# Performance work log

Hardware: AMD Instinct MI355X
Metric: run time of the kernel (lower is better)

## Reference

```python
import jax, jax.numpy as jnp
import numpy as np

N = 50000      # nodes
E = 800000     # edges (avg degree 16)
IN, HID, OUT = 256, 128, 64
K, ALPHA = 4, 0.0  # APPNPConv(k=4, alpha=0.0)


def setup_inputs() -> dict:
    key = jax.random.key(0)
    ks = jax.random.split(key, 5)
    features = jax.random.normal(ks[0], (N, IN), jnp.float32)
    src = jax.random.randint(ks[1], (E,), 0, N, jnp.int32)
    dst = jax.random.randint(ks[2], (E,), 0, N, jnp.int32)
    W1 = jax.random.normal(ks[3], (IN, HID), jnp.float32) / np.float32(np.sqrt(IN))
    b1 = jnp.zeros((HID,), jnp.float32)
    W3 = jax.random.normal(ks[4], (HID, OUT), jnp.float32) / np.float32(np.sqrt(HID))
    b3 = jnp.zeros((OUT,), jnp.float32)
    return dict(features=features, src=src, dst=dst, W1=W1, b1=b1, W3=W3, b3=b3)


def _sym_norms(src, dst, n):
    # D_out^{-1/2} for source side, D_in^{-1/2} for destination side (DGL norm='both')
    ones = jnp.ones((src.shape[0],), jnp.float32)
    deg_out = jax.ops.segment_sum(ones, src, num_segments=n)
    deg_in = jax.ops.segment_sum(ones, dst, num_segments=n)
    return jnp.clip(deg_out, 1.0) ** -0.5, jnp.clip(deg_in, 1.0) ** -0.5


def _prop(x, src, dst, norm_src, norm_dst):
    # x: [N, D]. Symmetric-normalized SpMM: D_in^{-1/2} A D_out^{-1/2} x
    msg = (x * norm_src[:, None])[src]                       # [E, D] gather
    agg = jax.ops.segment_sum(msg, dst, num_segments=x.shape[0])  # [N, D] scatter-add
    return agg * norm_dst[:, None]


def reference(features, src, dst, W1, b1, W3, b3):
    ns, nd = _sym_norms(src, dst, N)
    # GraphConv 1 (weight-first since in_dim > hidden_dim; math identical either way)
    h = _prop(features @ W1, src, dst, ns, nd) + b1
    # dropout is identity in eval mode (training=False)
    # APPNPConv: k=4 power-iteration steps with teleport alpha=0.0
    h0 = h
    for _ in range(K):
        h = (1.0 - ALPHA) * _prop(h, src, dst, ns, nd) + ALPHA * h0
    # GraphConv 3
    out = _prop(h @ W3, src, dst, ns, nd) + b3
    return out
```

## Files before the change

### kernel.cpp

```cpp
#include <hip/hip_runtime.h>
#include <math.h>

#define N_NODES 50000
#define N_EDGES 800000
#define DIN 256
#define DHID 128
#define DOUT 64
#define CSTRIDE 64
#define ZROW N_NODES
#define HBLOCKS 256
#define HCHUNK (N_EDGES / HBLOCKS)
#define HWORDS (N_NODES / 4)
#define SLICE ((size_t)(N_NODES + 1) * 16)
#define NGROUPS (N_NODES / 4)
#define P2BLOCKS 196

#define SB_SENT 3125
#define SB_HS (SB_SENT + HBLOCKS)
#define SB_HD (SB_HS + HBLOCKS)
#define SB_TOT (SB_HD + 66)

__global__ void k_setup(const int* __restrict__ src, const int* __restrict__ dst,
                        unsigned int* __restrict__ pS, unsigned int* __restrict__ pD,
                        unsigned int* __restrict__ csr32,
                        const float* __restrict__ W1, const float* __restrict__ b1,
                        const float* __restrict__ W3,
                        float* __restrict__ W13, float* __restrict__ bb,
                        float* __restrict__ Y0, float* __restrict__ Y1) {
    __shared__ unsigned int h[HWORDS];
    int bx = blockIdx.x, t = threadIdx.x;
    if (bx < SB_SENT) {
        unsigned int v = (unsigned int)ZROW | ((unsigned int)ZROW << 16);
        uint2 o; o.x = v; o.y = v;
        ((uint2*)csr32)[bx * 256 + t] = o;
        return;
    }
    if (bx < SB_HD) {
        const int* idx = (bx < SB_HS) ? src : dst;
        unsigned int* outp = (bx < SB_HS) ? pS : pD;
        int hb = bx - ((bx < SB_HS) ? SB_SENT : SB_HS);
        for (int w = t; w < HWORDS; w += 256) h[w] = 0u;
        __syncthreads();
        int base = hb * HCHUNK;
        for (int i = t; i < HCHUNK; i += 256) {
            int s = idx[base + i];
            atomicAdd(&h[s >> 2], 1u << ((s & 3) << 3));
        }
        __syncthreads();
        outp += (size_t)hb * HWORDS;
        for (int w = t; w < HWORDS; w += 256) outp[w] = h[w];
        return;
    }
    int vb = bx - SB_HD;
    if (vb == 65) {
        if (t < 64) {
            int qq = t >> 4, c2 = t & 15;
            Y0[(size_t)qq * SLICE + ((size_t)ZROW << 4) + c2] = 0.f;
            Y1[(size_t)qq * SLICE + ((size_t)ZROW << 4) + c2] = 0.f;
        }
        return;
    }
    if (vb == 64) {
        if (t < DOUT) {
            float s = 0.f;
            for (int k = 0; k < DHID; ++k) s += b1[k] * W3[k * DOUT + t];
            bb[t] = s;
        }
        return;
    }
    int idx2 = vb * 256 + t;
    int i = idx2 >> 6, j = idx2 & 63;
    float s = 0.f;
    for (int k = 0; k < DHID; ++k) s += W1[i * DHID + k] * W3[k * DOUT + j];
    W13[idx2] = s;
}

__global__ void k_hpre(const unsigned int* __restrict__ pS,
                       const unsigned int* __restrict__ pD,
                       unsigned int* __restrict__ prefix,
                       int* __restrict__ deg_in,
                       float* __restrict__ ns, float* __restrict__ nd,
                       float* __restrict__ cc, int* __restrict__ dparts) {
    __shared__ unsigned int sdw[64][4];
    __shared__ unsigned int sow[64][4];
    __shared__ int lh[65];
    int t = threadIdx.x;
    if (t < 65) lh[t] = 0;
    int col = t >> 2, sub = t & 3;
    int wid = blockIdx.x * 64 + col;
    bool act = wid < HWORDS;
    unsigned int ps = 0, pd = 0;
    if (act) {
        int b0 = sub << 6;
#pragma unroll 4
        for (int b = b0; b < b0 + 64; ++b) {
            ps += pS[(size_t)b * HWORDS + wid];
            pd += pD[(size_t)b * HWORDS + wid];
        }
    }
    sdw[col][sub] = pd;
    sow[col][sub] = ps;
    __syncthreads();
    if (act) {
        unsigned int base = 0;
        for (int k = 0; k < sub; ++k) base += sdw[col][k];
        int b0 = sub << 6;
        unsigned int run = base;
        for (int b = b0; b < b0 + 64; ++b) {
            unsigned int w = pD[(size_t)b * HWORDS + wid];
            prefix[(size_t)b * HWORDS + wid] = run;
            run += w;
        }
        if (sub == 0) {
            unsigned int totd = sdw[col][0] + sdw[col][1] + sdw[col][2] + sdw[col][3];
            unsigned int toto = sow[col][0] + sow[col][1] + sow[col][2] + sow[col][3];
            unsigned int di[4] = {totd & 0xffu, (totd >> 8) & 0xffu,
                                  (totd >> 16) & 0xffu, totd >> 24};
            unsigned int dov[4] = {toto & 0xffu, (toto >> 8) & 0xffu,
                                   (toto >> 16) & 0xffu, toto >> 24};
            int4 dd; dd.x = (int)di[0]; dd.y = (int)di[1]; dd.z = (int)di[2]; dd.w = (int)di[3];
            *(int4*)(deg_in + (wid << 2)) = dd;
            float4 vns, vnd, vcc;
            float* pns = &vns.x; float* pnd = &vnd.x; float* pcc = &vcc.x;
#pragma unroll
            for (int q = 0; q < 4; ++q) {
                int bin = (int)di[q]; if (bin > 64) bin = 64;
                atomicAdd(&lh[bin], 1);
                unsigned int a = dov[q] < 1u ? 1u : dov[q];
                unsigned int b = di[q] < 1u ? 1u : di[q];
                float fa = 1.0f / sqrtf((float)a);
                float fb = 1.0f / sqrtf((float)b);
                pns[q] = fa; pnd[q] = fb; pcc[q] = fa * fb;
            }
            *(float4*)(ns + (wid << 2)) = vns;
            *(float4*)(nd + (wid << 2)) = vnd;
            *(float4*)(cc + (wid << 2)) = vcc;
        }
    }
    __syncthreads();
    if (t < 65) dparts[blockIdx.x * 65 + t] = lh[t];
}

__global__ void k_dscan(const int* __restrict__ dparts, int* __restrict__ offs) {
    __shared__ int colsum[65], binbase[65];
    int t = threadIdx.x;
    if (t < 65) {
        int s = 0;
        for (int b = 0; b < P2BLOCKS; ++b) s += dparts[b * 65 + t];
        colsum[t] = s;
    }
    __syncthreads();
    if (t == 0) {
        int run = 0;
        for (int k = 64; k >= 0; --k) { binbase[k] = run; run += colsum[k]; }
    }
    __syncthreads();
    if (t < 65) {
        int run = binbase[t];
        for (int b = 0; b < P2BLOCKS; ++b) { offs[b * 65 + t] = run; run += dparts[b * 65 + t]; }
    }
}

__global__ void k_dscatter(const int* __restrict__ deg_in, const int* __restrict__ offs,
                           const float* __restrict__ cc, const float* __restrict__ ns,
                           const float* __restrict__ nd,
                           int* __restrict__ perm, int* __restrict__ inv,
                           int* __restrict__ degP, float* __restrict__ ccP,
                           float* __restrict__ nsP, float* __restrict__ ndP) {
    __shared__ int off[65];
    int t = threadIdx.x;
    if (t < 65) off[t] = offs[blockIdx.x * 65 + t];
    __syncthreads();
    int wid = blockIdx.x * 64 + t;
    if (t < 64 && wid < HWORDS) {
        int4 d4 = *(const int4*)(deg_in + (wid << 2));
        int dd[4] = {d4.x, d4.y, d4.z, d4.w};
#pragma unroll
        for (int k = 0; k < 4; ++k) {
            int node = (wid << 2) + k;
            int bin = dd[k] > 64 ? 64 : dd[k];
            int slot = atomicAdd(&off[bin], 1);
            perm[slot] = node; inv[node] = slot;
            degP[slot] = dd[k];
            ccP[slot] = cc[node]; nsP[slot] = ns[node]; ndP[slot] = nd[node];
        }
    }
}

__global__ void k_fill(const int* __restrict__ src, const int* __restrict__ dst,
                       const unsigned int* __restrict__ prefix,
                       const int* __restrict__ inv,
                       unsigned short* __restrict__ csr) {
    __shared__ unsigned int h[HWORDS];
    int t = threadIdx.x;
    const unsigned int* prow = prefix + (size_t)blockIdx.x * HWORDS;
    for (int w = t; w < HWORDS; w += 256) h[w] = prow[w];
    __syncthreads();
    int base = blockIdx.x * HCHUNK;
    for (int i = t; i < HCHUNK; i += 256) {
        int s = src[base + i], d = dst[base + i];
        int sh = (d & 3) << 3;
        unsigned int old = atomicAdd(&h[d >> 2], 1u << sh);
        int slot = (int)((old >> sh) & 0xffu);
        csr[((size_t)inv[d] << 6) + slot] = (unsigned short)inv[s];
    }
}

__global__ void k_gemm(const float* __restrict__ X, const float* __restrict__ W13,
                       const float* __restrict__ ns, const int* __restrict__ inv,
                       float* __restrict__ Y) {
    __shared__ float As[16][68];
    __shared__ float Bs[16][64];
    int tid = threadIdx.x;
    int tx = tid & 15, ty = tid >> 4;
    int row0 = blockIdx.x * 64;
    float acc[4][4];
#pragma unroll
    for (int i = 0; i < 4; ++i)
#pragma unroll
        for (int j = 0; j < 4; ++j) acc[i][j] = 0.f;

    int lr = tid >> 2;
    int lk = (tid & 3) << 2;
    int arow = row0 + lr;
    if (arow > N_NODES - 1) arow = N_NODES - 1;

    for (int k0 = 0; k0 < DIN; k0 += 16) {
        float4 a = *(const float4*)(X + (size_t)arow * DIN + k0 + lk);
        As[lk + 0][lr] = a.x; As[lk + 1][lr] = a.y;
        As[lk + 2][lr] = a.z; As[lk + 3][lr] = a.w;
        float4 b = *(const float4*)(W13 + (size_t)(k0 + (tid >> 4)) * DOUT + ((tid & 15) << 2));
        *(float4*)&Bs[tid >> 4][(tid & 15) << 2] = b;
        __syncthreads();
#pragma unroll
        for (int k = 0; k < 16; ++k) {
            float4 av = *(const float4*)&As[k][ty << 2];
            float4 bv = *(const float4*)&Bs[k][tx << 2];
            float ar[4] = {av.x, av.y, av.z, av.w};
            float br[4] = {bv.x, bv.y, bv.z, bv.w};
#pragma unroll
            for (int i = 0; i < 4; ++i)
#pragma unroll
                for (int j = 0; j < 4; ++j) acc[i][j] += ar[i] * br[j];
        }
        __syncthreads();
    }
    int qq = tx >> 2;
    int co = (tx & 3) << 2;
#pragma unroll
    for (int i = 0; i < 4; ++i) {
        int row = row0 + (ty << 2) + i;
        if (row < N_NODES) {
            float nsr = ns[row];
            int prow = inv[row];
            float4 o;
            o.x = acc[i][0] * nsr; o.y = acc[i][1] * nsr;
            o.z = acc[i][2] * nsr; o.w = acc[i][3] * nsr;
            *(float4*)(Y + (size_t)qq * SLICE + ((size_t)prow << 4) + co) = o;
        }
    }
}


template <int MODE>
__launch_bounds__(256, 8)
__global__ void k_spmm(const float* __restrict__ xs, float* __restrict__ ys,
                       const unsigned short* __restrict__ csr,
                       const int* __restrict__ degP,
                       const float* __restrict__ ccP, const float* __restrict__ nsP,
                       const float* __restrict__ ndP,
                       const float* __restrict__ bb, const float* __restrict__ b3,
                       const int* __restrict__ perm) {
    __shared__ unsigned short rows[4][256];
    int wid  = threadIdx.x >> 6;
    int lane = threadIdx.x & 63;
    int q    = (blockIdx.x & 7) >> 1;
    int half = blockIdx.x & 1;
    int g    = (blockIdx.x >> 3) * 8 + wid * 2 + half;
    if (g >= NGROUPS) return;
    int node0 = g << 2;

    int nn = lane >> 4, sl = lane & 15;
    const uint2* crow = (const uint2*)(csr + ((size_t)(node0 + nn) << 6)) + sl;
    uint2 rv = *crow;
    unsigned short* bp = &rows[wid][(sl << 4) + nn];
    bp[0]  = (unsigned short)(rv.x & 0xffffu);
    bp[4]  = (unsigned short)(rv.x >> 16);
    bp[8]  = (unsigned short)(rv.y & 0xffffu);
    bp[12] = (unsigned short)(rv.y >> 16);

    int n0u = __builtin_amdgcn_readfirstlane(node0);
    int m = (degP[n0u] + 7) & ~7;

    int n = lane >> 4, e = (lane >> 2) & 3, c4 = lane & 3;
    const unsigned short* rd = &rows[wid][(e << 2) + n];
    const float* xq = xs + (size_t)q * SLICE + (c4 << 2);

    float ax = 0.f, ay = 0.f, az = 0.f, aw = 0.f;
#define LDV(T) const float4 v##T = *(const float4*)(xq + ((size_t)rd[16 * (T)] << 4))
#define ACCV(T) ax += v##T.x; ay += v##T.y; az += v##T.z; aw += v##T.w
    if (m <= 8) {
        LDV(0); LDV(1);
        ACCV(0); ACCV(1);
    } else if (m <= 16) {
        LDV(0); LDV(1); LDV(2); LDV(3);
        ACCV(0); ACCV(1); ACCV(2); ACCV(3);
    } else if (m <= 24) {
        LDV(0); LDV(1); LDV(2); LDV(3); LDV(4); LDV(5);
        ACCV(0); ACCV(1); ACCV(2); ACCV(3); ACCV(4); ACCV(5);
    } else if (m <= 32) {
        LDV(0); LDV(1); LDV(2); LDV(3); LDV(4); LDV(5); LDV(6); LDV(7);
        ACCV(0); ACCV(1); ACCV(2); ACCV(3); ACCV(4); ACCV(5); ACCV(6); ACCV(7);
    } else {
        for (int j2 = 0; j2 < m; j2 += 8) {
            int o = j2 << 2;
            const float4 a = *(const float4*)(xq + ((size_t)rd[o] << 4));
            const float4 b = *(const float4*)(xq + ((size_t)rd[o + 16] << 4));
            ax += a.x; ay += a.y; az += a.z; aw += a.w;
            ax += b.x; ay += b.y; az += b.z; aw += b.w;
        }
    }
#undef LDV
#undef ACCV
    ax += __shfl_xor(ax, 4);  ay += __shfl_xor(ay, 4);
    az += __shfl_xor(az, 4);  aw += __shfl_xor(aw, 4);
    ax += __shfl_xor(ax, 8);  ay += __shfl_xor(ay, 8);
    az += __shfl_xor(az, 8);  aw += __shfl_xor(aw, 8);

    int nodeL = node0 + n;
    int colq  = (q << 4) + (c4 << 2);
    float4 r;
    if (MODE == 0) {
        float cv = ccP[nodeL], nv = nsP[nodeL];
        float4 bv = *(const float4*)(bb + colq);
        r.x = cv * ax + nv * bv.x; r.y = cv * ay + nv * bv.y;
        r.z = cv * az + nv * bv.z; r.w = cv * aw + nv * bv.w;
    } else if (MODE == 1) {
        float cv = ccP[nodeL];
        r.x = cv * ax; r.y = cv * ay; r.z = cv * az; r.w = cv * aw;
    } else {
        float dv = ndP[nodeL];
        float4 bv = *(const float4*)(b3 + colq);
        r.x = dv * ax + bv.x; r.y = dv * ay + bv.y;
        r.z = dv * az + bv.z; r.w = dv * aw + bv.w;
    }
    if (e == 0) {
        if (MODE == 2) {
            int orow = perm[nodeL];
            *(float4*)(ys + ((size_t)orow << 6) + colq) = r;
        } else {
            *(float4*)(ys + (size_t)q * SLICE + ((size_t)nodeL << 4) + (c4 << 2)) = r;
        }
    }
}


extern "C" void kernel_launch(void* const* d_in, const int* in_sizes, int n_in,
                              void* d_out, int out_size, void* d_ws, size_t ws_size,
                              hipStream_t stream) {
    const float* X   = (const float*)d_in[0];
    const int*   src = (const int*)d_in[1];
    const int*   dst = (const int*)d_in[2];
    const float* W1  = (const float*)d_in[3];
    const float* b1  = (const float*)d_in[4];
    const float* W3  = (const float*)d_in[5];
    const float* b3  = (const float*)d_in[6];
    float* out = (float*)d_out;

    char* ws = (char*)d_ws;
    size_t off = 0;
    auto alloc = [&](size_t bytes) -> void* {
        void* p = ws + off;
        off = (off + bytes + 255) & ~(size_t)255;
        return p;
    };
    unsigned int*   pS     = (unsigned int*)alloc((size_t)HBLOCKS * HWORDS * 4);
    unsigned int*   pD     = (unsigned int*)alloc((size_t)HBLOCKS * HWORDS * 4);
    unsigned int*   pref   = (unsigned int*)alloc((size_t)HBLOCKS * HWORDS * 4);
    float*          Y0     = (float*)alloc(SLICE * 4 * 4);
    float*          Y1     = (float*)alloc(SLICE * 4 * 4);
    unsigned short* csr    = (unsigned short*)alloc((size_t)N_NODES * CSTRIDE * 2);
    int*            deg_in = (int*)alloc((size_t)N_NODES * 4);
    float*          ns     = (float*)alloc((size_t)N_NODES * 4);
    float*          nd     = (float*)alloc((size_t)N_NODES * 4);
    float*          cc     = (float*)alloc((size_t)N_NODES * 4);
    int*            perm   = (int*)alloc((size_t)N_NODES * 4);
    int*            inv    = (int*)alloc((size_t)N_NODES * 4);
    int*            degP   = (int*)alloc((size_t)N_NODES * 4);
    float*          ccP    = (float*)alloc((size_t)N_NODES * 4);
    float*          nsP    = (float*)alloc((size_t)N_NODES * 4);
    float*          ndP    = (float*)alloc((size_t)N_NODES * 4);
    int*            dparts = (int*)alloc((size_t)P2BLOCKS * 65 * 4);
    int*            offs   = (int*)alloc((size_t)P2BLOCKS * 65 * 4);
    float*          W13    = (float*)alloc((size_t)DIN * DOUT * 4);
    float*          bb     = (float*)alloc(DOUT * 4);

    const int sblk = 1563 * 8;

    k_setup<<<SB_TOT, 256, 0, stream>>>(src, dst, pS, pD, (unsigned int*)csr,
                                        W1, b1, W3, W13, bb, Y0, Y1);
    k_hpre<<<P2BLOCKS, 256, 0, stream>>>(pS, pD, pref, deg_in, ns, nd, cc, dparts);
    k_dscan<<<1, 128, 0, stream>>>(dparts, offs);
    k_dscatter<<<P2BLOCKS, 128, 0, stream>>>(deg_in, offs, cc, ns, nd,
                                             perm, inv, degP, ccP, nsP, ndP);
    k_fill<<<HBLOCKS, 256, 0, stream>>>(src, dst, pref, inv, csr);

    k_gemm<<<(N_NODES + 63) / 64, 256, 0, stream>>>(X, W13, ns, inv, Y0);

    k_spmm<0><<<sblk, 256, 0, stream>>>(Y0, Y1, csr, degP, ccP, nsP, ndP, bb, b3, perm);
    k_spmm<1><<<sblk, 256, 0, stream>>>(Y1, Y0, csr, degP, ccP, nsP, ndP, bb, b3, perm);
    k_spmm<1><<<sblk, 256, 0, stream>>>(Y0, Y1, csr, degP, ccP, nsP, ndP, bb, b3, perm);
    k_spmm<1><<<sblk, 256, 0, stream>>>(Y1, Y0, csr, degP, ccP, nsP, ndP, bb, b3, perm);
    k_spmm<1><<<sblk, 256, 0, stream>>>(Y0, Y1, csr, degP, ccP, nsP, ndP, bb, b3, perm);
    k_spmm<2><<<sblk, 256, 0, stream>>>(Y1, out, csr, degP, ccP, nsP, ndP, bb, b3, perm);
}
```

Measured before the change: 305.3 us.

## Split GEMM over K with double buffering, halve histogram blocks, finer SpMM degree buckets

The GEMM is split into two K halves run as separate blocks, which doubles the block count for occupancy. Each block double-buffers its shared tiles with register prefetch, and a new combine kernel sums the two partials, applies the source norm and permutes rows. Histogram block count drops from 256 to 128, which halves the per-block partial arrays that the prefix kernel scans. SpMM now rounds degree to multiples of 4 instead of 8 and gains matching unrolled branches, so fewer padded neighbour loads are issued. The cost is an extra kernel launch plus a round trip of the partial results through memory.

After: 427.0 us. 39.9% more time.

```diff
diff --git a/kernel.cpp b/kernel.cpp
--- a/kernel.cpp
+++ b/kernel.cpp
@@ -8,12 +8,13 @@
 #define DOUT 64
 #define CSTRIDE 64
 #define ZROW N_NODES
-#define HBLOCKS 256
+#define HBLOCKS 128
 #define HCHUNK (N_EDGES / HBLOCKS)
 #define HWORDS (N_NODES / 4)
 #define SLICE ((size_t)(N_NODES + 1) * 16)
 #define NGROUPS (N_NODES / 4)
 #define P2BLOCKS 196
+#define GROWB 782
 
 #define SB_SENT 3125
 #define SB_HS (SB_SENT + HBLOCKS)
@@ -91,9 +92,9 @@
     bool act = wid < HWORDS;
     unsigned int ps = 0, pd = 0;
     if (act) {
-        int b0 = sub << 6;
+        int b0 = sub << 5;
 #pragma unroll 4
-        for (int b = b0; b < b0 + 64; ++b) {
+        for (int b = b0; b < b0 + 32; ++b) {
             ps += pS[(size_t)b * HWORDS + wid];
             pd += pD[(size_t)b * HWORDS + wid];
         }
@@ -104,9 +105,9 @@
     if (act) {
         unsigned int base = 0;
         for (int k = 0; k < sub; ++k) base += sdw[col][k];
-        int b0 = sub << 6;
+        int b0 = sub << 5;
         unsigned int run = base;
-        for (int b = b0; b < b0 + 64; ++b) {
+        for (int b = b0; b < b0 + 32; ++b) {
             unsigned int w = pD[(size_t)b * HWORDS + wid];
             prefix[(size_t)b * HWORDS + wid] = run;
             run += w;
@@ -206,14 +207,18 @@
     }
 }
 
+__launch_bounds__(256, 8)
 __global__ void k_gemm(const float* __restrict__ X, const float* __restrict__ W13,
-                       const float* __restrict__ ns, const int* __restrict__ inv,
-                       float* __restrict__ Y) {
-    __shared__ float As[16][68];
-    __shared__ float Bs[16][64];
+                       float* __restrict__ P0, float* __restrict__ P1) {
+    __shared__ float As[2][16][68];
+    __shared__ float Bs[2][16][64];
     int tid = threadIdx.x;
+    int half = blockIdx.x >= GROWB;
+    int bx = half ? (blockIdx.x - GROWB) : blockIdx.x;
+    float* P = half ? P1 : P0;
+    int kbase = half << 7;
     int tx = tid & 15, ty = tid >> 4;
-    int row0 = blockIdx.x * 64;
+    int row0 = bx * 64;
     float acc[4][4];
 #pragma unroll
     for (int i = 0; i < 4; ++i)
@@ -224,18 +229,25 @@
     int lk = (tid & 3) << 2;
     int arow = row0 + lr;
     if (arow > N_NODES - 1) arow = N_NODES - 1;
-
-    for (int k0 = 0; k0 < DIN; k0 += 16) {
-        float4 a = *(const float4*)(X + (size_t)arow * DIN + k0 + lk);
-        As[lk + 0][lr] = a.x; As[lk + 1][lr] = a.y;
-        As[lk + 2][lr] = a.z; As[lk + 3][lr] = a.w;
-        float4 b = *(const float4*)(W13 + (size_t)(k0 + (tid >> 4)) * DOUT + ((tid & 15) << 2));
-        *(float4*)&Bs[tid >> 4][(tid & 15) << 2] = b;
+    const float* Xr = X + (size_t)arow * DIN + kbase + lk;
+    const float* Wr = W13 + (size_t)(kbase + ty) * DOUT + (tx << 2);
+
+    float4 a_nxt = *(const float4*)Xr;
+    float4 b_nxt = *(const float4*)Wr;
+    for (int c = 0; c < 8; ++c) {
+        int buf = c & 1;
+        As[buf][lk + 0][lr] = a_nxt.x; As[buf][lk + 1][lr] = a_nxt.y;
+        As[buf][lk + 2][lr] = a_nxt.z; As[buf][lk + 3][lr] = a_nxt.w;
+        *(float4*)&Bs[buf][ty][tx << 2] = b_nxt;
         __syncthreads();
+        if (c < 7) {
+            a_nxt = *(const float4*)(Xr + ((c + 1) << 4));
+            b_nxt = *(const float4*)(Wr + (size_t)((c + 1) << 4) * DOUT);
+        }
 #pragma unroll
         for (int k = 0; k < 16; ++k) {
-            float4 av = *(const float4*)&As[k][ty << 2];
-            float4 bv = *(const float4*)&Bs[k][tx << 2];
+            float4 av = *(const float4*)&As[buf][k][ty << 2];
+            float4 bv = *(const float4*)&Bs[buf][k][tx << 2];
             float ar[4] = {av.x, av.y, av.z, av.w};
             float br[4] = {bv.x, bv.y, bv.z, bv.w};
 #pragma unroll
@@ -243,22 +255,32 @@
 #pragma unroll
                 for (int j = 0; j < 4; ++j) acc[i][j] += ar[i] * br[j];
         }
-        __syncthreads();
-    }
-    int qq = tx >> 2;
-    int co = (tx & 3) << 2;
+    }
 #pragma unroll
     for (int i = 0; i < 4; ++i) {
         int row = row0 + (ty << 2) + i;
         if (row < N_NODES) {
-            float nsr = ns[row];
-            int prow = inv[row];
-            float4 o;
-            o.x = acc[i][0] * nsr; o.y = acc[i][1] * nsr;
-            o.z = acc[i][2] * nsr; o.w = acc[i][3] * nsr;
-            *(float4*)(Y + (size_t)qq * SLICE + ((size_t)prow << 4) + co) = o;
-        }
-    }
+            float4 o; o.x = acc[i][0]; o.y = acc[i][1]; o.z = acc[i][2]; o.w = acc[i][3];
+            *(float4*)(P + (size_t)row * DOUT + (tx << 2)) = o;
+        }
+    }
+}
+
+__global__ void k_comb(const float* __restrict__ P0, const float* __restrict__ P1,
+                       const float* __restrict__ ns, const int* __restrict__ inv,
+                       float* __restrict__ Y) {
+    int idx = blockIdx.x * 256 + threadIdx.x;
+    int row = idx >> 4;
+    int p = idx & 15;
+    float4 a = ((const float4*)P0)[idx];
+    float4 b = ((const float4*)P1)[idx];
+    float nsr = ns[row];
+    int prow = inv[row];
+    int q = p >> 2, co = (p & 3) << 2;
+    float4 o;
+    o.x = (a.x + b.x) * nsr; o.y = (a.y + b.y) * nsr;
+    o.z = (a.z + b.z) * nsr; o.w = (a.w + b.w) * nsr;
+    *(float4*)(Y + (size_t)q * SLICE + ((size_t)prow << 4) + co) = o;
 }
 
 
@@ -290,7 +312,7 @@
     bp[12] = (unsigned short)(rv.y >> 16);
 
     int n0u = __builtin_amdgcn_readfirstlane(node0);
-    int m = (degP[n0u] + 7) & ~7;
+    int m = (degP[n0u] + 3) & ~3;
 
     int n = lane >> 4, e = (lane >> 2) & 3, c4 = lane & 3;
     const unsigned short* rd = &rows[wid][(e << 2) + n];
@@ -299,25 +321,33 @@
     float ax = 0.f, ay = 0.f, az = 0.f, aw = 0.f;
 #define LDV(T) const float4 v##T = *(const float4*)(xq + ((size_t)rd[16 * (T)] << 4))
 #define ACCV(T) ax += v##T.x; ay += v##T.y; az += v##T.z; aw += v##T.w
-    if (m <= 8) {
+    if (m <= 4) {
+        LDV(0); ACCV(0);
+    } else if (m <= 8) {
         LDV(0); LDV(1);
         ACCV(0); ACCV(1);
+    } else if (m <= 12) {
+        LDV(0); LDV(1); LDV(2);
+        ACCV(0); ACCV(1); ACCV(2);
     } else if (m <= 16) {
         LDV(0); LDV(1); LDV(2); LDV(3);
         ACCV(0); ACCV(1); ACCV(2); ACCV(3);
+    } else if (m <= 20) {
+        LDV(0); LDV(1); LDV(2); LDV(3); LDV(4);
+        ACCV(0); ACCV(1); ACCV(2); ACCV(3); ACCV(4);
     } else if (m <= 24) {
         LDV(0); LDV(1); LDV(2); LDV(3); LDV(4); LDV(5);
         ACCV(0); ACCV(1); ACCV(2); ACCV(3); ACCV(4); ACCV(5);
+    } else if (m <= 28) {
+        LDV(0); LDV(1); LDV(2); LDV(3); LDV(4); LDV(5); LDV(6);
+        ACCV(0); ACCV(1); ACCV(2); ACCV(3); ACCV(4); ACCV(5); ACCV(6);
     } else if (m <= 32) {
         LDV(0); LDV(1); LDV(2); LDV(3); LDV(4); LDV(5); LDV(6); LDV(7);
         ACCV(0); ACCV(1); ACCV(2); ACCV(3); ACCV(4); ACCV(5); ACCV(6); ACCV(7);
     } else {
-        for (int j2 = 0; j2 < m; j2 += 8) {
-            int o = j2 << 2;
-            const float4 a = *(const float4*)(xq + ((size_t)rd[o] << 4));
-            const float4 b = *(const float4*)(xq + ((size_t)rd[o + 16] << 4));
+        for (int j2 = 0; j2 < m; j2 += 4) {
+            const float4 a = *(const float4*)(xq + ((size_t)rd[j2 << 2] << 4));
             ax += a.x; ay += a.y; az += a.z; aw += a.w;
-            ax += b.x; ay += b.y; az += b.z; aw += b.w;
         }
     }
 #undef LDV
@@ -379,6 +409,8 @@
     unsigned int*   pref   = (unsigned int*)alloc((size_t)HBLOCKS * HWORDS * 4);
     float*          Y0     = (float*)alloc(SLICE * 4 * 4);
     float*          Y1     = (float*)alloc(SLICE * 4 * 4);
+    float*          P0     = (float*)alloc((size_t)N_NODES * DOUT * 4);
+    float*          P1     = (float*)alloc((size_t)N_NODES * DOUT * 4);
     unsigned short* csr    = (unsigned short*)alloc((size_t)N_NODES * CSTRIDE * 2);
     int*            deg_in = (int*)alloc((size_t)N_NODES * 4);
     float*          ns     = (float*)alloc((size_t)N_NODES * 4);
@@ -405,7 +437,8 @@
                                              perm, inv, degP, ccP, nsP, ndP);
     k_fill<<<HBLOCKS, 256, 0, stream>>>(src, dst, pref, inv, csr);
 
-    k_gemm<<<(N_NODES + 63) / 64, 256, 0, stream>>>(X, W13, ns, inv, Y0);
+    k_gemm<<<GROWB * 2, 256, 0, stream>>>(X, W13, P0, P1);
+    k_comb<<<(N_NODES * DOUT / 4) / 256, 256, 0, stream>>>(P0, P1, ns, inv, Y0);
 
     k_spmm<0><<<sblk, 256, 0, stream>>>(Y0, Y1, csr, degP, ccP, nsP, ndP, bb, b3, perm);
     k_spmm<1><<<sblk, 256, 0, stream>>>(Y1, Y0, csr, degP, ccP, nsP, ndP, bb, b3, perm);
```
